# Performance work log

Hardware: AMD Instinct MI355X
Metric: run time of the kernel (lower is better)

Reference implementation:

```python
import jax, jax.numpy as jnp
import numpy as np
import math

B, N, T_LEN, K, H, W, SH, HID = 8, 64, 1024, 12, 8, 8, 9, 32


def _normalize(x, axis, eps):
    n = jnp.linalg.norm(x, axis=axis, keepdims=True)
    return x / jnp.maximum(n, eps)


def _camera_plane_basis(L):
    # L: (B,K,3,T) unit vectors -> orthonormal image-plane basis e1,e2 (B,K,3,T)
    a1 = jnp.broadcast_to(jnp.array([1.0, 0.0, 0.0], L.dtype).reshape(1, 1, 3, 1), L.shape)
    a2 = jnp.broadcast_to(jnp.array([0.0, 1.0, 0.0], L.dtype).reshape(1, 1, 3, 1), L.shape)
    e1 = jnp.cross(L, a1, axis=2)
    small = jnp.linalg.norm(e1, axis=2, keepdims=True) < 1e-4
    e1 = jnp.where(small, jnp.cross(L, a2, axis=2), e1)
    e1 = _normalize(e1, 2, 1e-6)
    e2 = _normalize(jnp.cross(e1, L, axis=2), 2, 1e-6)
    return e1, e2


def _lead_cnn(x, w1, b1, w2, b2, wf, bf):
    # x: (B*T, 2, H, W) -> (B*T, 1); GELU is exact (erf) as in torch nn.GELU()
    dn = ('NCHW', 'OIHW', 'NCHW')
    h = jax.lax.conv_general_dilated(x, w1, (1, 1), 'SAME', dimension_numbers=dn) + b1[None, :, None, None]
    h = jax.nn.gelu(h, approximate=False)
    h = jax.lax.conv_general_dilated(h, w2, (1, 1), 'SAME', dimension_numbers=dn) + b2[None, :, None, None]
    h = jax.nn.gelu(h, approximate=False)
    h = h.mean(axis=(2, 3))  # AdaptiveAvgPool2d(1) + flatten
    return h @ wf.T + bf[None, :]


def _forward(mu, sigma0, sigma_vel, amplitude, sh_base, sh_vel, p0, p_vel,
             chest_offset, resp_freq, resp_vec,
             splat_tau_raw, limb_ra, limb_la, limb_ll, chest_vectors,
             w1, b1, w2, b2, wf, bf, T):
    Bb, Nn = mu.shape
    gx = jnp.linspace(-1.0, 1.0, W, dtype=mu.dtype).reshape(1, 1, 1, 1, W)
    gy = jnp.linspace(-1.0, 1.0, H, dtype=mu.dtype).reshape(1, 1, 1, H, 1)
    t = jnp.linspace(0.0, 1.0, T, dtype=mu.dtype).reshape(1, 1, T)
    dt = t - mu[:, :, None]                                          # (B,N,T)
    sigma_t = jax.nn.softplus(sigma0[:, :, None] + sigma_vel[:, :, None] * dt) + 1e-3
    gauss = amplitude[:, :, None] * jnp.exp(-0.5 * (dt / sigma_t) ** 2)   # (B,N,T)
    sh_dyn = sh_base[:, :, :, None] + sh_vel[:, :, :, None] * dt[:, :, None, :]  # (B,N,9,T)
    p_t = p0[:, :, :, None] + p_vel[:, :, :, None] * dt[:, :, None, :]           # (B,N,3,T)
    p_hat = _normalize(p_t, 2, 1e-6)
    # limb lead axes derived from RA/LA/LL triangle
    L_I = _normalize(limb_la - limb_ra, -1, 1e-6)
    L_II = _normalize(limb_ll - limb_ra, -1, 1e-6)
    L_III = _normalize(limb_ll - limb_la, -1, 1e-6)
    L_aVR = _normalize(limb_ra - (limb_la + limb_ll) * 0.5, -1, 1e-6)
    L_aVL = _normalize(limb_la - (limb_ra + limb_ll) * 0.5, -1, 1e-6)
    L_aVF = _normalize(limb_ll - (limb_ra + limb_la) * 0.5, -1, 1e-6)
    limb = jnp.stack([L_I, L_II, L_III, L_aVR, L_aVL, L_aVF], axis=0)  # (6,3)
    chest = _normalize(chest_vectors, -1, 1e-12)
    chest_p = _normalize(chest[None] + chest_offset, -1, 1e-12)        # (B,6,3)
    lead_vecs = jnp.concatenate([jnp.broadcast_to(limb[None], (Bb, 6, 3)), chest_p], axis=1)  # (B,12,3)
    lead_vecs_t = jnp.broadcast_to(lead_vecs[..., None], (Bb, K, 3, T))
    osc = resp_vec.reshape(Bb, 1, 3, 1) * jnp.sin(2.0 * jnp.pi * resp_freq.reshape(Bb, 1, 1, 1) * t.reshape(1, 1, 1, T))
    lead_vecs_t = _normalize(lead_vecs_t + osc, 2, 1e-12)              # (B,12,3,T)
    e1, e2 = _camera_plane_basis(lead_vecs_t)
    u = jnp.tanh(jnp.einsum('bnct,bkct->bnkt', p_hat, e1))            # (B,N,12,T)
    v = jnp.tanh(jnp.einsum('bnct,bkct->bnkt', p_hat, e2))
    x_lv, y_lv, z_lv = lead_vecs_t[:, :, 0, :], lead_vecs_t[:, :, 1, :], lead_vecs_t[:, :, 2, :]
    Y = jnp.stack([0.282095 * jnp.ones_like(x_lv), -0.488603 * y_lv, 0.488603 * z_lv, -0.488603 * x_lv,
                   1.092548 * x_lv * y_lv, -1.092548 * y_lv * z_lv, 0.315392 * (3.0 * z_lv ** 2 - 1.0),
                   -1.092548 * x_lv * z_lv, 0.546274 * (x_lv ** 2 - y_lv ** 2)], axis=2)  # (B,12,9,T)
    sh_proj = jnp.einsum('bnmt,bkmt->bnkt', sh_dyn, Y)                # (B,N,12,T)
    tau = jax.nn.softplus(splat_tau_raw) + 0.06
    cosp = jnp.einsum('bnct,bkct->bnkt', p_hat, lead_vecs_t)          # (B,N,12,T)

    # splat accumulation: scan over N gaussians (memory-bound rasterization)
    def body(carry, xs):
        sp, ss = carry
        u_n, v_n, g_n, sh_n, c_n = xs   # (B,12,T),(B,12,T),(B,T),(B,12,T),(B,12,T)
        du = u_n[..., None, None] - gx  # (B,12,T,1,W)
        dv = v_n[..., None, None] - gy  # (B,12,T,H,1)
        kernel = jnp.exp(-0.5 * (du * du + dv * dv) / (tau * tau))  # (B,12,T,H,W)
        hem = jnp.maximum(c_n, 0.0)[..., None, None]  # half-space gate
        sp = sp + g_n[:, None, :, None, None] * kernel * hem
        ss = ss + (g_n[:, None, :] * sh_n)[..., None, None] * kernel * hem
        return (sp, ss), None

    body = jax.checkpoint(body)
    init = (jnp.zeros((Bb, K, T, H, W), mu.dtype), jnp.zeros((Bb, K, T, H, W), mu.dtype))
    xs = (jnp.moveaxis(u, 1, 0), jnp.moveaxis(v, 1, 0), jnp.moveaxis(gauss, 1, 0),
          jnp.moveaxis(sh_proj, 1, 0), jnp.moveaxis(cosp, 1, 0))
    (splat_pos, splat_sh), _ = jax.lax.scan(body, init, xs)

    # per-lead CNN decode; replicate torch's cat(dim=1)+reshape semantics exactly
    outs = []
    for k in range(K):
        cat = jnp.concatenate([splat_pos[:, k], splat_sh[:, k]], axis=1)  # (B,2T,H,W)
        inp = cat.reshape(Bb * T, 2, H, W)
        outs.append(_lead_cnn(inp, w1[k], b1[k], w2[k], b2[k], wf[k], bf[k]))  # (B*T,1)
    V = jnp.concatenate(outs, axis=1).reshape(Bb, K, T)  # matches torch .view(B,12,T)
    return V


def setup_inputs() -> dict:
    key = jax.random.key(0)
    ks = jax.random.split(key, 16)
    f32 = jnp.float32
    mu = jax.random.uniform(ks[0], (B, N), f32)
    sigma0 = jax.random.normal(ks[1], (B, N), f32) * 0.5
    sigma_vel = jax.random.normal(ks[2], (B, N), f32) * 0.1
    amplitude = jax.random.normal(ks[3], (B, N), f32)
    sh_base = jax.random.normal(ks[4], (B, N, SH), f32) * 0.5
    sh_vel = jax.random.normal(ks[5], (B, N, SH), f32) * 0.1
    p0 = jax.random.normal(ks[6], (B, N, 3), f32)
    p_vel = jax.random.normal(ks[7], (B, N, 3), f32) * 0.1
    chest_offset = jax.random.normal(ks[8], (B, 6, 3), f32) * 0.1
    resp_freq = jax.random.uniform(ks[9], (B,), f32, 0.1, 0.5)
    resp_vec = jax.random.normal(ks[10], (B, 3), f32) * 0.1
    # learned parameters at their torch init values
    splat_tau_raw = jnp.zeros((), f32)
    limb_ra = jnp.zeros((3,), f32)
    limb_la = jnp.array([1.0, 0.0, 0.0], f32)
    limb_ll = jnp.array([0.5, math.sqrt(3.0) / 2.0, 0.0], f32)
    raw = np.array([[-0.707, 0.0, 0.707], [0.0, 0.0, 1.0], [0.438, 0.0, 0.899],
                    [0.707, 0.0, 0.707], [0.899, 0.0, 0.438], [0.966, 0.0, 0.259]], np.float32)
    chest_vectors = jnp.asarray(raw / np.linalg.norm(raw, axis=-1, keepdims=True))
    w1 = jax.random.normal(ks[11], (K, HID, 2, 3, 3), f32) * 0.1
    b1 = jnp.zeros((K, HID), f32)
    w2 = jax.random.normal(ks[12], (K, HID, HID, 3, 3), f32) * 0.05
    b2 = jnp.zeros((K, HID), f32)
    wf = jax.random.normal(ks[13], (K, 1, HID), f32) * 0.1
    bf = jnp.zeros((K, 1), f32)
    return dict(mu=mu, sigma0=sigma0, sigma_vel=sigma_vel, amplitude=amplitude,
                sh_base=sh_base, sh_vel=sh_vel, p0=p0, p_vel=p_vel,
                chest_offset=chest_offset, resp_freq=resp_freq, resp_vec=resp_vec,
                splat_tau_raw=splat_tau_raw, limb_ra=limb_ra, limb_la=limb_la, limb_ll=limb_ll,
                chest_vectors=chest_vectors, w1=w1, b1=b1, w2=w2, b2=b2, wf=wf, bf=bf, T=T_LEN)


def reference(mu, sigma0, sigma_vel, amplitude, sh_base, sh_vel, p0, p_vel,
              chest_offset, resp_freq, resp_vec,
              splat_tau_raw, limb_ra, limb_la, limb_ll, chest_vectors,
              w1, b1, w2, b2, wf, bf, T):
    return _forward(mu, sigma0, sigma_vel, amplitude, sh_base, sh_vel, p0, p_vel,
                    chest_offset, resp_freq, resp_vec,
                    splat_tau_raw, limb_ra, limb_la, limb_ll, chest_vectors,
                    w1, b1, w2, b2, wf, bf, int(T))
```

## Files before the change

### kernel.cpp

```cpp
#include <hip/hip_runtime.h>
#include <hip/hip_bf16.h>
#include <math.h>

#define BB 8
#define NN 64
#define TT 1024
#define KK 12
#define BKT (BB*KK*TT)
#define W2SS 2312

#define WAVE_FENCE() asm volatile("" ::: "memory")

typedef short bf16x8 __attribute__((ext_vector_type(8)));
typedef float f32x4  __attribute__((ext_vector_type(4)));

__device__ __forceinline__ float fast_rcp(float x)  { return __builtin_amdgcn_rcpf(x); }
__device__ __forceinline__ float fast_exp2(float x) { return __builtin_amdgcn_exp2f(x); }
__device__ __forceinline__ float fast_log2(float x) { return __builtin_amdgcn_logf(x); }

__device__ __forceinline__ float fast_softplus(float x) {
    float a = fabsf(x);
    float e = fast_exp2(-1.44269504f * a);
    float l = fast_log2(1.0f + e) * 0.69314718f;
    return fmaxf(x, 0.0f) + l;
}
__device__ __forceinline__ float fast_tanh(float x) {
    float t = fast_exp2(x * 2.885390082f);
    return fmaf(-2.0f, fast_rcp(t + 1.0f), 1.0f);
}
__device__ __forceinline__ float fast_erf(float x) {
    float ax = fabsf(x);
    float t  = fast_rcp(fmaf(0.3275911f, ax, 1.0f));
    float p  = fmaf(fmaf(fmaf(fmaf(1.061405429f, t, -1.453152027f), t,
                   1.421413741f), t, -0.284496736f), t, 0.254829592f) * t;
    float e  = fast_exp2(-1.44269504f * ax * ax);
    float r  = fmaf(-p, e, 1.0f);
    return copysignf(r, x);
}
__device__ __forceinline__ float fast_gelu(float x) {
    return 0.5f * x * (1.0f + fast_erf(x * 0.70710678118654752f));
}
__device__ __forceinline__ short f2bf(float x) {
    return (short)__builtin_bit_cast(unsigned short, __float2bfloat16(x));
}

__global__ void prep_lead(const float* __restrict__ chest_offset,
                          const float* __restrict__ resp_freq,
                          const float* __restrict__ resp_vec,
                          const float* __restrict__ limb_ra,
                          const float* __restrict__ limb_la,
                          const float* __restrict__ limb_ll,
                          const float* __restrict__ chest_vectors,
                          float* __restrict__ lead)
{
    int id = blockIdx.x * blockDim.x + threadIdx.x;
    if (id >= BKT) return;
    int t  = id & (TT - 1);
    int bk = id >> 10;
    int k  = bk % KK;
    int b  = bk / KK;

    float lx, ly, lz;
    if (k < 6) {
        float rax = limb_ra[0], ray = limb_ra[1], raz = limb_ra[2];
        float lax = limb_la[0], lay = limb_la[1], laz = limb_la[2];
        float llx = limb_ll[0], lly = limb_ll[1], llz = limb_ll[2];
        float dx, dy, dz;
        switch (k) {
            case 0: dx = lax - rax; dy = lay - ray; dz = laz - raz; break;
            case 1: dx = llx - rax; dy = lly - ray; dz = llz - raz; break;
            case 2: dx = llx - lax; dy = lly - lay; dz = llz - laz; break;
            case 3: dx = rax - 0.5f*(lax+llx); dy = ray - 0.5f*(lay+lly); dz = raz - 0.5f*(laz+llz); break;
            case 4: dx = lax - 0.5f*(rax+llx); dy = lay - 0.5f*(ray+lly); dz = laz - 0.5f*(raz+llz); break;
            default:dx = llx - 0.5f*(rax+lax); dy = lly - 0.5f*(ray+lay); dz = llz - 0.5f*(raz+laz); break;
        }
        float n   = sqrtf(dx*dx + dy*dy + dz*dz);
        float inv = 1.0f / fmaxf(n, 1e-6f);
        lx = dx*inv; ly = dy*inv; lz = dz*inv;
    } else {
        int j = k - 6;
        float cx = chest_vectors[j*3+0], cy = chest_vectors[j*3+1], cz = chest_vectors[j*3+2];
        float n   = sqrtf(cx*cx + cy*cy + cz*cz);
        float inv = 1.0f / fmaxf(n, 1e-12f);
        cx *= inv; cy *= inv; cz *= inv;
        cx += chest_offset[(b*6+j)*3+0];
        cy += chest_offset[(b*6+j)*3+1];
        cz += chest_offset[(b*6+j)*3+2];
        n   = sqrtf(cx*cx + cy*cy + cz*cz);
        inv = 1.0f / fmaxf(n, 1e-12f);
        lx = cx*inv; ly = cy*inv; lz = cz*inv;
    }

    float tl = t * (1.0f / (TT - 1));
    float ph = 6.283185307179586f * resp_freq[b] * tl;
    float sv = sinf(ph);
    float Lx = lx + resp_vec[b*3+0] * sv;
    float Ly = ly + resp_vec[b*3+1] * sv;
    float Lz = lz + resp_vec[b*3+2] * sv;
    float n   = sqrtf(Lx*Lx + Ly*Ly + Lz*Lz);
    float inv = 1.0f / fmaxf(n, 1e-12f);
    Lx *= inv; Ly *= inv; Lz *= inv;

    float e1x = 0.0f, e1y = Lz, e1z = -Ly;
    float n1  = sqrtf(e1y*e1y + e1z*e1z);
    if (n1 < 1e-4f) { e1x = -Lz; e1y = 0.0f; e1z = Lx; }
    float ne1 = sqrtf(e1x*e1x + e1y*e1y + e1z*e1z);
    inv = 1.0f / fmaxf(ne1, 1e-6f);
    e1x *= inv; e1y *= inv; e1z *= inv;

    float e2x = e1y*Lz - e1z*Ly;
    float e2y = e1z*Lx - e1x*Lz;
    float e2z = e1x*Ly - e1y*Lx;
    float ne2 = sqrtf(e2x*e2x + e2y*e2y + e2z*e2z);
    inv = 1.0f / fmaxf(ne2, 1e-6f);
    e2x *= inv; e2y *= inv; e2z *= inv;

    lead[ 0*BKT + id] = Lx;
    lead[ 1*BKT + id] = Ly;
    lead[ 2*BKT + id] = Lz;
    lead[ 3*BKT + id] = e1x;
    lead[ 4*BKT + id] = e1y;
    lead[ 5*BKT + id] = e1z;
    lead[ 6*BKT + id] = e2x;
    lead[ 7*BKT + id] = e2y;
    lead[ 8*BKT + id] = e2z;
    lead[ 9*BKT + id] = 0.282095f;
    lead[10*BKT + id] = -0.488603f * Ly;
    lead[11*BKT + id] =  0.488603f * Lz;
    lead[12*BKT + id] = -0.488603f * Lx;
    lead[13*BKT + id] =  1.092548f * Lx * Ly;
    lead[14*BKT + id] = -1.092548f * Ly * Lz;
    lead[15*BKT + id] =  0.315392f * (3.0f * Lz * Lz - 1.0f);
    lead[16*BKT + id] = -1.092548f * Lx * Lz;
    lead[17*BKT + id] =  0.546274f * (Lx * Lx - Ly * Ly);
}

__global__ void prep_w2bf(const float* __restrict__ w2, unsigned short* __restrict__ out)
{
    int id = blockIdx.x * blockDim.x + threadIdx.x;
    if (id >= KK*4*9*32*8) return;
    int j   = id & 7;
    int r1  = id >> 3;
    int oc  = r1 & 31;
    int r2  = r1 >> 5;
    int tap = r2 % 9;
    int r3  = r2 / 9;
    int kc  = r3 & 3;
    int k   = r3 >> 2;
    float v = w2[((k*32 + oc)*32 + (kc*8 + j))*9 + tap];
    out[id] = __builtin_bit_cast(unsigned short, __float2bfloat16(v));
}

__global__ __launch_bounds__(256, 3) void fused_main(
    const float* __restrict__ mu,       const float* __restrict__ sigma0,
    const float* __restrict__ sigma_vel,const float* __restrict__ amplitude,
    const float* __restrict__ sh_base,  const float* __restrict__ sh_vel,
    const float* __restrict__ p0,       const float* __restrict__ p_vel,
    const float* __restrict__ tau_raw,
    const float* __restrict__ w1,       const float* __restrict__ b1,
    const unsigned short* __restrict__ w2bf, const float* __restrict__ b2,
    const float* __restrict__ wf,       const float* __restrict__ bfp,
    const float* __restrict__ lead,     float* __restrict__ out)
{
    __shared__ __align__(16) short  w2s[4*W2SS];
    __shared__ __align__(16) short  h1c[4][3200];
    __shared__ __align__(16) float4 qbuf[4][2][64];

    const int wave = threadIdx.x >> 6;
    const int lane = threadIdx.x & 63;
    const int bid  = blockIdx.x;
    const int ig   = bid & 127;
    const int k    = (bid >> 7) % KK;
    const int b    = bid / (128 * KK);
    const int i    = ig * 4 + wave;
    const int t0   = 2 * i;

    {
        const unsigned* w2u = (const unsigned*)(w2bf + k * 9216);
        for (int idx = threadIdx.x; idx < 4608; idx += 256) {
            unsigned v = w2u[idx];
            int sp  = idx << 1;
            int kc  = sp / 2304;
            int rem = sp - kc * 2304;
            *(unsigned*)&w2s[kc * W2SS + rem] = v;
        }
    }
    {
        unsigned* hz = (unsigned*)&h1c[wave][0];
        #pragma unroll
        for (int j = 0; j < 25; ++j) hz[lane + j*64] = 0u;
    }
    __syncthreads();

    {
        const int n  = lane;
        const int bn = b * NN + n;
        const float muv = mu[bn], s0v = sigma0[bn], svv = sigma_vel[bn], amp = amplitude[bn];
        const float p0x = p0[bn*3+0], p0y = p0[bn*3+1], p0z = p0[bn*3+2];
        const float pvx = p_vel[bn*3+0], pvy = p_vel[bn*3+1], pvz = p_vel[bn*3+2];
        float shb[9], shv[9];
        #pragma unroll
        for (int m = 0; m < 9; ++m) { shb[m] = sh_base[bn*9+m]; shv[m] = sh_vel[bn*9+m]; }

        #pragma unroll
        for (int tt = 0; tt < 2; ++tt) {
            const int t  = t0 + tt;
            const int li = (b*KK + k)*TT + t;
            const float Lx  = lead[0*BKT+li], Ly  = lead[1*BKT+li], Lz  = lead[2*BKT+li];
            const float e1x = lead[3*BKT+li], e1y = lead[4*BKT+li], e1z = lead[5*BKT+li];
            const float e2x = lead[6*BKT+li], e2y = lead[7*BKT+li], e2z = lead[8*BKT+li];
            float Yv[9];
            #pragma unroll
            for (int m = 0; m < 9; ++m) Yv[m] = lead[(9+m)*BKT + li];

            const float tl = t * (1.0f / (TT - 1));
            const float dt = tl - muv;
            const float sig = fast_softplus(s0v + svv*dt) + 0.001f;
            const float z   = dt * fast_rcp(sig);
            const float g   = amp * fast_exp2(-0.721347520f * z * z);
            float px = p0x + pvx*dt, py = p0y + pvy*dt, pz = p0z + pvz*dt;
            const float pn   = sqrtf(px*px + py*py + pz*pz);
            const float pinv = fast_rcp(fmaxf(pn, 1e-6f));
            px *= pinv; py *= pinv; pz *= pinv;
            const float u    = fast_tanh(px*e1x + py*e1y + pz*e1z);
            const float v    = fast_tanh(px*e2x + py*e2y + pz*e2z);
            const float hem  = fmaxf(px*Lx + py*Ly + pz*Lz, 0.0f);
            const float a    = g * hem;
            float shp = 0.0f;
            #pragma unroll
            for (int m = 0; m < 9; ++m) shp = fmaf(fmaf(shv[m], dt, shb[m]), Yv[m], shp);
            qbuf[wave][tt][n] = make_float4(u, v, a, a * shp);
        }
    }
    WAVE_FENCE();

    const int h = lane >> 3, w = lane & 7;
    const int ppix = (h + 1) * 10 + (w + 1);
    const float gx = -1.0f + w * (2.0f / 7.0f);
    const float gy = -1.0f + h * (2.0f / 7.0f);
    const float tau = fast_softplus(tau_raw[0]) + 0.06f;
    const float fl2 = -0.721347520f * fast_rcp(tau * tau);

    float pos0 = 0.0f, pos1 = 0.0f, shp0 = 0.0f, shp1 = 0.0f;
    #pragma unroll 4
    for (int n = 0; n < 64; ++n) {
        float4 q0 = qbuf[wave][0][n];
        float du = q0.x - gx, dv = q0.y - gy;
        float e  = fast_exp2(fl2 * (du*du + dv*dv));
        pos0 = fmaf(q0.z, e, pos0); shp0 = fmaf(q0.w, e, shp0);
        float4 q1 = qbuf[wave][1][n];
        du = q1.x - gx; dv = q1.y - gy;
        e  = fast_exp2(fl2 * (du*du + dv*dv));
        pos1 = fmaf(q1.z, e, pos1); shp1 = fmaf(q1.w, e, shp1);
    }
    WAVE_FENCE();

    float* inbw = (float*)&qbuf[wave][0][0];
    #pragma unroll
    for (int j = 0; j < 7; ++j) {
        int idx = lane + j*64;
        if (idx < 400) inbw[idx] = 0.0f;
    }
    inbw[  0 + ppix] = pos0;
    inbw[100 + ppix] = pos1;
    inbw[200 + ppix] = shp0;
    inbw[300 + ppix] = shp1;
    WAVE_FENCE();

    const float* w1p = w1 + k*32*2*9;
    const int g  = lane >> 4;
    const int r15 = lane & 15;
    float b2v[8], wfv[8];
    #pragma unroll
    for (int mt = 0; mt < 2; ++mt)
        #pragma unroll
        for (int r = 0; r < 4; ++r) {
            int oc = mt*16 + g*4 + r;
            b2v[mt*4+r] = b2[k*32 + oc];
            wfv[mt*4+r] = wf[k*32 + oc];
        }
    const float bfv = bfp[k];

    short* h1w = &h1c[wave][0];
    float results[2];

    #pragma unroll
    for (int s = 0; s < 2; ++s) {
        float g1[32];
        {
            float nb[18];
            #pragma unroll
            for (int ch = 0; ch < 2; ++ch)
                #pragma unroll
                for (int tap = 0; tap < 9; ++tap)
                    nb[ch*9+tap] = inbw[(2*s+ch)*100 + ppix + (tap/3 - 1)*10 + (tap%3 - 1)];
            #pragma unroll
            for (int oc = 0; oc < 32; ++oc) {
                float acc = b1[k*32 + oc];
                #pragma unroll
                for (int q = 0; q < 18; ++q)
                    acc = fmaf(w1p[oc*18 + q], nb[q], acc);
                g1[oc] = fast_gelu(acc);
            }
        }
        #pragma unroll
        for (int kc = 0; kc < 4; ++kc) {
            bf16x8 v;
            #pragma unroll
            for (int j = 0; j < 8; ++j) v[j] = f2bf(g1[kc*8 + j]);
            *(bf16x8*)&h1w[kc*800 + ppix*8] = v;
        }
        WAVE_FENCE();

        f32x4 acc[2][4];
        #pragma unroll
        for (int mt = 0; mt < 2; ++mt)
            #pragma unroll
            for (int nt = 0; nt < 4; ++nt) acc[mt][nt] = (f32x4)0.0f;

        const short* w2g = &w2s[g * W2SS];
        const short* h1g = &h1w[g * 800];
        const int prow0 = (lane >> 3) & 1;
        const int pb    = (prow0 + 1)*10 + (lane & 7) + 1;

        #pragma unroll
        for (int tap = 0; tap < 9; ++tap) {
            const int dy = tap/3 - 1, dx = tap%3 - 1;
            bf16x8 a0 = *(const bf16x8*)&w2g[(tap*32 +      r15)*8];
            bf16x8 a1 = *(const bf16x8*)&w2g[(tap*32 + 16 + r15)*8];
            const short* bp = &h1g[(pb + dy*10 + dx)*8];
            bf16x8 bv0 = *(const bf16x8*)&bp[0];
            bf16x8 bv1 = *(const bf16x8*)&bp[160];
            bf16x8 bv2 = *(const bf16x8*)&bp[320];
            bf16x8 bv3 = *(const bf16x8*)&bp[480];
            acc[0][0] = __builtin_amdgcn_mfma_f32_16x16x32_bf16(a0, bv0, acc[0][0], 0, 0, 0);
            acc[1][0] = __builtin_amdgcn_mfma_f32_16x16x32_bf16(a1, bv0, acc[1][0], 0, 0, 0);
            acc[0][1] = __builtin_amdgcn_mfma_f32_16x16x32_bf16(a0, bv1, acc[0][1], 0, 0, 0);
            acc[1][1] = __builtin_amdgcn_mfma_f32_16x16x32_bf16(a1, bv1, acc[1][1], 0, 0, 0);
            acc[0][2] = __builtin_amdgcn_mfma_f32_16x16x32_bf16(a0, bv2, acc[0][2], 0, 0, 0);
            acc[1][2] = __builtin_amdgcn_mfma_f32_16x16x32_bf16(a1, bv2, acc[1][2], 0, 0, 0);
            acc[0][3] = __builtin_amdgcn_mfma_f32_16x16x32_bf16(a0, bv3, acc[0][3], 0, 0, 0);
            acc[1][3] = __builtin_amdgcn_mfma_f32_16x16x32_bf16(a1, bv3, acc[1][3], 0, 0, 0);
        }
        WAVE_FENCE();

        float p = 0.0f;
        #pragma unroll
        for (int mt = 0; mt < 2; ++mt)
            #pragma unroll
            for (int nt = 0; nt < 4; ++nt)
                #pragma unroll
                for (int r = 0; r < 4; ++r)
                    p = fmaf(fast_gelu(acc[mt][nt][r] + b2v[mt*4+r]), wfv[mt*4+r], p);
        #pragma unroll
        for (int off = 32; off >= 1; off >>= 1)
            p += __shfl_xor(p, off, 64);
        results[s] = bfv + p * (1.0f / 64.0f);
    }

    if (lane == 0) {
        out[(b*TT + i      ) * KK + k] = results[0];
        out[(b*TT + i + 512) * KK + k] = results[1];
    }
}

extern "C" void kernel_launch(void* const* d_in, const int* in_sizes, int n_in,
                              void* d_out, int out_size, void* d_ws, size_t ws_size,
                              hipStream_t stream)
{
    const float* mu            = (const float*)d_in[0];
    const float* sigma0        = (const float*)d_in[1];
    const float* sigma_vel     = (const float*)d_in[2];
    const float* amplitude     = (const float*)d_in[3];
    const float* sh_base       = (const float*)d_in[4];
    const float* sh_vel        = (const float*)d_in[5];
    const float* p0            = (const float*)d_in[6];
    const float* p_vel         = (const float*)d_in[7];
    const float* chest_offset  = (const float*)d_in[8];
    const float* resp_freq     = (const float*)d_in[9];
    const float* resp_vec      = (const float*)d_in[10];
    const float* tau_raw       = (const float*)d_in[11];
    const float* limb_ra       = (const float*)d_in[12];
    const float* limb_la       = (const float*)d_in[13];
    const float* limb_ll       = (const float*)d_in[14];
    const float* chest_vectors = (const float*)d_in[15];
    const float* w1            = (const float*)d_in[16];
    const float* b1            = (const float*)d_in[17];
    const float* w2            = (const float*)d_in[18];
    const float* b2            = (const float*)d_in[19];
    const float* wf            = (const float*)d_in[20];
    const float* bfp           = (const float*)d_in[21];

    float*          lead = (float*)d_ws;
    unsigned short* w2bf = (unsigned short*)(lead + 18*BKT);

    hipLaunchKernelGGL(prep_lead, dim3(BKT/256), dim3(256), 0, stream,
                       chest_offset, resp_freq, resp_vec,
                       limb_ra, limb_la, limb_ll, chest_vectors, lead);
    hipLaunchKernelGGL(prep_w2bf, dim3((KK*4*9*32*8 + 255)/256), dim3(256), 0, stream, w2, w2bf);
    hipLaunchKernelGGL(fused_main, dim3(BB*KK*128), dim3(256), 0, stream,
                       mu, sigma0, sigma_vel, amplitude, sh_base, sh_vel, p0, p_vel,
                       tau_raw, w1, b1, w2bf, b2, wf, bfp, lead, (float*)d_out);
}
```

Baseline: 539.1 us.

## Replace padded LDS staging with shuffles, masked unpadded conv2 layout, higher occupancy

Conv1 inputs are now gathered from neighbouring lanes with cross-lane shuffles instead of being written to a zero-padded 10x10 LDS plane. The conv2 activation buffer moves from a padded layout to an unpadded 64-pixel layout with an XOR swizzle, so it no longer needs zeroing. Out-of-range taps are handled with per-lane bitmasks applied to the MFMA operands, and the bias b2 is folded into the accumulator initialisation. Per-wave LDS shrinks and launch bounds rise from 3 to 4 blocks per CU, trading extra masking ALU work and possible register pressure for occupancy.

```diff
diff --git a/kernel.cpp b/kernel.cpp
--- a/kernel.cpp
+++ b/kernel.cpp
@@ -13,6 +13,7 @@
 
 typedef short bf16x8 __attribute__((ext_vector_type(8)));
 typedef float f32x4  __attribute__((ext_vector_type(4)));
+typedef int   i32x4  __attribute__((ext_vector_type(4)));
 
 __device__ __forceinline__ float fast_rcp(float x)  { return __builtin_amdgcn_rcpf(x); }
 __device__ __forceinline__ float fast_exp2(float x) { return __builtin_amdgcn_exp2f(x); }
@@ -151,7 +152,7 @@
     out[id] = __builtin_bit_cast(unsigned short, __float2bfloat16(v));
 }
 
-__global__ __launch_bounds__(256, 3) void fused_main(
+__global__ __launch_bounds__(256, 4) void fused_main(
     const float* __restrict__ mu,       const float* __restrict__ sigma0,
     const float* __restrict__ sigma_vel,const float* __restrict__ amplitude,
     const float* __restrict__ sh_base,  const float* __restrict__ sh_vel,
@@ -162,9 +163,8 @@
     const float* __restrict__ wf,       const float* __restrict__ bfp,
     const float* __restrict__ lead,     float* __restrict__ out)
 {
-    __shared__ __align__(16) short  w2s[4*W2SS];
-    __shared__ __align__(16) short  h1c[4][3200];
-    __shared__ __align__(16) float4 qbuf[4][2][64];
+    __shared__ __align__(16) short w2s[4*W2SS];
+    __shared__ __align__(16) short Uw[4][2048];
 
     const int wave = threadIdx.x >> 6;
     const int lane = threadIdx.x & 63;
@@ -174,6 +174,8 @@
     const int b    = bid / (128 * KK);
     const int i    = ig * 4 + wave;
     const int t0   = 2 * i;
+    const int r15  = lane & 15;
+    const int g    = lane >> 4;
 
     {
         const unsigned* w2u = (const unsigned*)(w2bf + k * 9216);
@@ -185,13 +187,9 @@
             *(unsigned*)&w2s[kc * W2SS + rem] = v;
         }
     }
-    {
-        unsigned* hz = (unsigned*)&h1c[wave][0];
-        #pragma unroll
-        for (int j = 0; j < 25; ++j) hz[lane + j*64] = 0u;
-    }
     __syncthreads();
 
+    float4* qb = (float4*)&Uw[wave][0];
     {
         const int n  = lane;
         const int bn = b * NN + n;
@@ -217,7 +215,7 @@
             const float dt = tl - muv;
             const float sig = fast_softplus(s0v + svv*dt) + 0.001f;
             const float z   = dt * fast_rcp(sig);
-            const float g   = amp * fast_exp2(-0.721347520f * z * z);
+            const float gss = amp * fast_exp2(-0.721347520f * z * z);
             float px = p0x + pvx*dt, py = p0y + pvy*dt, pz = p0z + pvz*dt;
             const float pn   = sqrtf(px*px + py*py + pz*pz);
             const float pinv = fast_rcp(fmaxf(pn, 1e-6f));
@@ -225,17 +223,16 @@
             const float u    = fast_tanh(px*e1x + py*e1y + pz*e1z);
             const float v    = fast_tanh(px*e2x + py*e2y + pz*e2z);
             const float hem  = fmaxf(px*Lx + py*Ly + pz*Lz, 0.0f);
-            const float a    = g * hem;
+            const float a    = gss * hem;
             float shp = 0.0f;
             #pragma unroll
             for (int m = 0; m < 9; ++m) shp = fmaf(fmaf(shv[m], dt, shb[m]), Yv[m], shp);
-            qbuf[wave][tt][n] = make_float4(u, v, a, a * shp);
+            qb[tt*64 + n] = make_float4(u, v, a, a * shp);
         }
     }
     WAVE_FENCE();
 
     const int h = lane >> 3, w = lane & 7;
-    const int ppix = (h + 1) * 10 + (w + 1);
     const float gx = -1.0f + w * (2.0f / 7.0f);
     const float gy = -1.0f + h * (2.0f / 7.0f);
     const float tau = fast_softplus(tau_raw[0]) + 0.06f;
@@ -244,32 +241,19 @@
     float pos0 = 0.0f, pos1 = 0.0f, shp0 = 0.0f, shp1 = 0.0f;
     #pragma unroll 4
     for (int n = 0; n < 64; ++n) {
-        float4 q0 = qbuf[wave][0][n];
+        float4 q0 = qb[n];
         float du = q0.x - gx, dv = q0.y - gy;
         float e  = fast_exp2(fl2 * (du*du + dv*dv));
         pos0 = fmaf(q0.z, e, pos0); shp0 = fmaf(q0.w, e, shp0);
-        float4 q1 = qbuf[wave][1][n];
+        float4 q1 = qb[64 + n];
         du = q1.x - gx; dv = q1.y - gy;
         e  = fast_exp2(fl2 * (du*du + dv*dv));
         pos1 = fmaf(q1.z, e, pos1); shp1 = fmaf(q1.w, e, shp1);
     }
     WAVE_FENCE();
 
-    float* inbw = (float*)&qbuf[wave][0][0];
-    #pragma unroll
-    for (int j = 0; j < 7; ++j) {
-        int idx = lane + j*64;
-        if (idx < 400) inbw[idx] = 0.0f;
-    }
-    inbw[  0 + ppix] = pos0;
-    inbw[100 + ppix] = pos1;
-    inbw[200 + ppix] = shp0;
-    inbw[300 + ppix] = shp1;
-    WAVE_FENCE();
-
     const float* w1p = w1 + k*32*2*9;
-    const int g  = lane >> 4;
-    const int r15 = lane & 15;
+    const float* b1p = b1 + k*32;
     float b2v[8], wfv[8];
     #pragma unroll
     for (int mt = 0; mt < 2; ++mt)
@@ -281,66 +265,85 @@
         }
     const float bfv = bfp[k];
 
-    short* h1w = &h1c[wave][0];
+    unsigned mval[4];
+    #pragma unroll
+    for (int nt = 0; nt < 4; ++nt) {
+        const int pix = r15 + nt*16;
+        const int ph2 = pix >> 3, pw2 = pix & 7;
+        unsigned m = 0;
+        #pragma unroll
+        for (int tap = 0; tap < 9; ++tap) {
+            const int dy = tap/3 - 1, dx = tap%3 - 1;
+            m |= ((((unsigned)(ph2 + dy)) < 8u) & (((unsigned)(pw2 + dx)) < 8u)) ? (1u << tap) : 0u;
+        }
+        mval[nt] = m;
+    }
+
+    short* h1w = &Uw[wave][0];
+    const int swz = (lane >> 1) & 3;
     float results[2];
 
     #pragma unroll
     for (int s = 0; s < 2; ++s) {
-        float g1[32];
-        {
-            float nb[18];
-            #pragma unroll
-            for (int ch = 0; ch < 2; ++ch)
-                #pragma unroll
-                for (int tap = 0; tap < 9; ++tap)
-                    nb[ch*9+tap] = inbw[(2*s+ch)*100 + ppix + (tap/3 - 1)*10 + (tap%3 - 1)];
-            #pragma unroll
-            for (int oc = 0; oc < 32; ++oc) {
-                float acc = b1[k*32 + oc];
-                #pragma unroll
-                for (int q = 0; q < 18; ++q)
-                    acc = fmaf(w1p[oc*18 + q], nb[q], acc);
-                g1[oc] = fast_gelu(acc);
-            }
-        }
-        #pragma unroll
-        for (int kc = 0; kc < 4; ++kc) {
-            bf16x8 v;
-            #pragma unroll
-            for (int j = 0; j < 8; ++j) v[j] = f2bf(g1[kc*8 + j]);
-            *(bf16x8*)&h1w[kc*800 + ppix*8] = v;
-        }
-        WAVE_FENCE();
-
-        f32x4 acc[2][4];
-        #pragma unroll
-        for (int mt = 0; mt < 2; ++mt)
-            #pragma unroll
-            for (int nt = 0; nt < 4; ++nt) acc[mt][nt] = (f32x4)0.0f;
-
-        const short* w2g = &w2s[g * W2SS];
-        const short* h1g = &h1w[g * 800];
-        const int prow0 = (lane >> 3) & 1;
-        const int pb    = (prow0 + 1)*10 + (lane & 7) + 1;
-
+        const float c0 = (s == 0) ? pos0 : shp0;
+        const float c1 = (s == 0) ? pos1 : shp1;
+        float nb[18];
         #pragma unroll
         for (int tap = 0; tap < 9; ++tap) {
             const int dy = tap/3 - 1, dx = tap%3 - 1;
+            const int nl = lane + dy*8 + dx;
+            const bool valid = (((unsigned)(h + dy)) < 8u) & (((unsigned)(w + dx)) < 8u);
+            float v0 = __shfl(c0, nl, 64);
+            float v1 = __shfl(c1, nl, 64);
+            nb[tap]     = valid ? v0 : 0.0f;
+            nb[9 + tap] = valid ? v1 : 0.0f;
+        }
+        float g1[32];
+        #pragma unroll
+        for (int oc = 0; oc < 32; ++oc) {
+            float acc = b1p[oc];
+            #pragma unroll
+            for (int q = 0; q < 18; ++q)
+                acc = fmaf(w1p[oc*18 + q], nb[q], acc);
+            g1[oc] = fast_gelu(acc);
+        }
+        #pragma unroll
+        for (int q = 0; q < 4; ++q) {
+            bf16x8 v;
+            #pragma unroll
+            for (int j = 0; j < 8; ++j) v[j] = f2bf(g1[q*8 + j]);
+            *(bf16x8*)&h1w[lane*32 + ((q ^ swz) * 8)] = v;
+        }
+        WAVE_FENCE();
+
+        f32x4 acc[2][4];
+        #pragma unroll
+        for (int mt = 0; mt < 2; ++mt) {
+            f32x4 binit;
+            #pragma unroll
+            for (int r = 0; r < 4; ++r) binit[r] = b2v[mt*4+r];
+            #pragma unroll
+            for (int nt = 0; nt < 4; ++nt) acc[mt][nt] = binit;
+        }
+        const short* w2g = &w2s[g * W2SS];
+        #pragma unroll
+        for (int tap = 0; tap < 9; ++tap) {
+            const int dy = tap/3 - 1, dx = tap%3 - 1;
+            const int D  = dy*8 + dx;
             bf16x8 a0 = *(const bf16x8*)&w2g[(tap*32 +      r15)*8];
             bf16x8 a1 = *(const bf16x8*)&w2g[(tap*32 + 16 + r15)*8];
-            const short* bp = &h1g[(pb + dy*10 + dx)*8];
-            bf16x8 bv0 = *(const bf16x8*)&bp[0];
-            bf16x8 bv1 = *(const bf16x8*)&bp[160];
-            bf16x8 bv2 = *(const bf16x8*)&bp[320];
-            bf16x8 bv3 = *(const bf16x8*)&bp[480];
-            acc[0][0] = __builtin_amdgcn_mfma_f32_16x16x32_bf16(a0, bv0, acc[0][0], 0, 0, 0);
-            acc[1][0] = __builtin_amdgcn_mfma_f32_16x16x32_bf16(a1, bv0, acc[1][0], 0, 0, 0);
-            acc[0][1] = __builtin_amdgcn_mfma_f32_16x16x32_bf16(a0, bv1, acc[0][1], 0, 0, 0);
-            acc[1][1] = __builtin_amdgcn_mfma_f32_16x16x32_bf16(a1, bv1, acc[1][1], 0, 0, 0);
-            acc[0][2] = __builtin_amdgcn_mfma_f32_16x16x32_bf16(a0, bv2, acc[0][2], 0, 0, 0);
-            acc[1][2] = __builtin_amdgcn_mfma_f32_16x16x32_bf16(a1, bv2, acc[1][2], 0, 0, 0);
-            acc[0][3] = __builtin_amdgcn_mfma_f32_16x16x32_bf16(a0, bv3, acc[0][3], 0, 0, 0);
-            acc[1][3] = __builtin_amdgcn_mfma_f32_16x16x32_bf16(a1, bv3, acc[1][3], 0, 0, 0);
+            #pragma unroll
+            for (int nt = 0; nt < 4; ++nt) {
+                const int spix = (r15 + nt*16 + D) & 63;
+                const int q2   = g ^ ((spix >> 1) & 3);
+                bf16x8 bv = *(const bf16x8*)&h1w[spix*32 + q2*8];
+                const unsigned msk = ((mval[nt] >> tap) & 1u) ? 0xFFFFFFFFu : 0u;
+                i32x4 bi = __builtin_bit_cast(i32x4, bv);
+                bi[0] &= msk; bi[1] &= msk; bi[2] &= msk; bi[3] &= msk;
+                bv = __builtin_bit_cast(bf16x8, bi);
+                acc[0][nt] = __builtin_amdgcn_mfma_f32_16x16x32_bf16(a0, bv, acc[0][nt], 0, 0, 0);
+                acc[1][nt] = __builtin_amdgcn_mfma_f32_16x16x32_bf16(a1, bv, acc[1][nt], 0, 0, 0);
+            }
         }
         WAVE_FENCE();
 
@@ -351,7 +354,7 @@
             for (int nt = 0; nt < 4; ++nt)
                 #pragma unroll
                 for (int r = 0; r < 4; ++r)
-                    p = fmaf(fast_gelu(acc[mt][nt][r] + b2v[mt*4+r]), wfv[mt*4+r], p);
+                    p = fmaf(fast_gelu(acc[mt][nt][r]), wfv[mt*4+r], p);
         #pragma unroll
         for (int off = 32; off >= 1; off >>= 1)
             p += __shfl_xor(p, off, 64);
```

Result: slower. 552.1 us (+2.4%).
